# Kernel optimization log

Hardware: AMD Instinct MI355X
Metric: run time of the kernel (lower is better)

The kernel has to match this reference:

```python
import jax, jax.numpy as jnp
import numpy as np

N = 4096
STEPS = 100


def setup_inputs() -> dict:
    key = jax.random.key(0)
    k1, k2 = jax.random.split(key)
    z = jax.random.normal(k1, (N, 2), dtype=jnp.float32) * 0.1  # points in the disc
    K = jax.random.normal(k2, (N, N), dtype=jnp.float32) * 0.1  # coupling matrix param
    omega = jnp.float32(0.1)  # learned natural frequency (scalar)
    dt = jnp.float32(0.05)
    return {"z": z, "K": K, "omega": omega, "dt": dt, "steps": STEPS}


def reference(z, K, omega, dt, steps):
    n = z.shape[0]
    inv2n = 1.0 / (2.0 * n)
    z_c = jax.lax.complex(z[:, 0], z[:, 1])          # (N,) complex64
    K_c = K.astype(jnp.complex64)                    # (N,N) complex (zero imag part)

    def step(zc, _):
        S = K_c @ jnp.conj(zc)                       # (N,)
        T = K_c @ zc                                 # (N,)
        dz = -inv2n * S * zc**2 + omega * zc + inv2n * T
        zc = zc + dt * dz
        a = jnp.abs(zc)
        mask = a >= 0.999
        safe_a = jnp.where(mask, a, 1.0)             # avoid div-by-zero in untaken branch
        zc = jnp.where(mask, zc / safe_a * 0.999, zc)
        return zc, None

    z_c, _ = jax.lax.scan(step, z_c, None, length=steps)

    z_final = jnp.stack([jnp.real(z_c), jnp.imag(z_c)], axis=1)  # (N,2)
    norms = jnp.linalg.norm(z_final, axis=1, keepdims=True)
    mask = norms >= 0.999
    safe_n = jnp.where(mask, norms, 1.0)
    z_final = jnp.where(mask, z_final / safe_n * 0.999, z_final)
    return z_final
```

## Files before the change

### kernel.cpp

```cpp
#include <hip/hip_runtime.h>

#define NN 4096
#define NSTEPS 100
#define TPB 512
#define NBLK 256

__device__ __forceinline__ void zstore_u64(float2* p, unsigned long long u) {
    __hip_atomic_store((unsigned long long*)p, u, __ATOMIC_RELAXED,
                       __HIP_MEMORY_SCOPE_AGENT);
}
__device__ __forceinline__ unsigned long long zload_u64(const float2* p) {
    return __hip_atomic_load((const unsigned long long*)p, __ATOMIC_RELAXED,
                             __HIP_MEMORY_SCOPE_AGENT);
}

__global__ __launch_bounds__(TPB, 2) void k_persist(
    const float* __restrict__ K, const float2* __restrict__ z0,
    float2* __restrict__ zb0, float2* __restrict__ zb1,
    float2* __restrict__ zfinal, const float* __restrict__ omega_p,
    const float* __restrict__ dt_p) {
    __shared__ float P[2][8][68];

    const int tid  = threadIdx.x;
    const int bid  = blockIdx.x;
    const int w    = tid >> 6, lane = tid & 63;
    const int colbase = w * 512 + lane;

    const float omega = *omega_p;
    const float dt    = *dt_p;
    const float inv2n = 1.0f / (2.0f * NN);

    float kA[16][8];
#pragma unroll
    for (int r = 0; r < 16; ++r) {
        const float* Kr = K + (size_t)(bid * 16 + r) * NN + colbase;
#pragma unroll
        for (int j = 0; j < 8; ++j) kA[r][j] = Kr[j * 64];
    }

    float x = 0.f, y = 0.f;
    if ((lane & 31) == 0) {
        float2 zc = z0[bid * 16 + 2 * w + (lane >> 5)];
        x = zc.x; y = zc.y;
    }

    unsigned long long v[8];

    for (int s = 0; s < NSTEPS; ++s) {
#pragma unroll
        for (int r = 0; r < 16; ++r)
#pragma unroll
            for (int j = 0; j < 8; ++j) asm volatile("" : "+v"(kA[r][j]));

        float zre[8], zim[8];
        if (s == 0) {
#pragma unroll
            for (int j = 0; j < 8; ++j) {
                float2 zc = z0[colbase + j * 64];
                zre[j] = zc.x; zim[j] = zc.y;
            }
        } else {
            const float2* zsrc = (s & 1) ? zb1 : zb0;
            const unsigned tag = (unsigned)(s & 7);
            unsigned stale = 0u;
#pragma unroll
            for (int j = 0; j < 8; ++j)
                stale |= (((unsigned)v[j] & 7u) != tag) ? (1u << j) : 0u;
            while (stale) {
                __builtin_amdgcn_s_sleep(1);
#pragma unroll
                for (int j = 0; j < 8; ++j)
                    if (stale & (1u << j))
                        v[j] = zload_u64(zsrc + colbase + j * 64);
#pragma unroll
                for (int j = 0; j < 8; ++j)
                    if ((stale & (1u << j)) && ((unsigned)v[j] & 7u) == tag)
                        stale &= ~(1u << j);
            }
#pragma unroll
            for (int j = 0; j < 8; ++j) {
                union { unsigned u; float f; } cx, cy;
                cx.u = (unsigned)v[j];
                cy.u = (unsigned)(v[j] >> 32);
                zre[j] = cx.f; zim[j] = cy.f;
            }
        }

        float sr[16], si[16];
#pragma unroll
        for (int r = 0; r < 16; ++r) { sr[r] = 0.f; si[r] = 0.f; }
#pragma unroll
        for (int j = 0; j < 8; ++j) {
#pragma unroll
            for (int r = 0; r < 16; ++r) {
                sr[r] += kA[r][j] * zre[j];
                si[r] += kA[r][j] * zim[j];
            }
        }

        if (s + 1 < NSTEPS) {
            const float2* zn = ((s + 1) & 1) ? zb1 : zb0;
#pragma unroll
            for (int j = 0; j < 8; ++j)
                v[j] = zload_u64(zn + colbase + j * 64);
        }

        float a32[32];
#pragma unroll
        for (int r = 0; r < 16; ++r) { a32[r] = sr[r]; a32[16 + r] = si[r]; }
        float b16[16];
#pragma unroll
        for (int m = 0; m < 16; ++m) {
            float aa = a32[2 * m], bb = a32[2 * m + 1];
            bool hi = lane & 1;
            float snd = hi ? aa : bb, kp = hi ? bb : aa;
            b16[m] = kp + __shfl_xor(snd, 1, 64);
        }
        float b8[8];
#pragma unroll
        for (int m = 0; m < 8; ++m) {
            float aa = b16[2 * m], bb = b16[2 * m + 1];
            bool hi = lane & 2;
            float snd = hi ? aa : bb, kp = hi ? bb : aa;
            b8[m] = kp + __shfl_xor(snd, 2, 64);
        }
        float b4[4];
#pragma unroll
        for (int m = 0; m < 4; ++m) {
            float aa = b8[2 * m], bb = b8[2 * m + 1];
            bool hi = lane & 4;
            float snd = hi ? aa : bb, kp = hi ? bb : aa;
            b4[m] = kp + __shfl_xor(snd, 4, 64);
        }
        float b2[2];
#pragma unroll
        for (int m = 0; m < 2; ++m) {
            float aa = b4[2 * m], bb = b4[2 * m + 1];
            bool hi = lane & 8;
            float snd = hi ? aa : bb, kp = hi ? bb : aa;
            b2[m] = kp + __shfl_xor(snd, 8, 64);
        }
        {
            float aa = b2[0], bb = b2[1];
            bool hi = lane & 16;
            float snd = hi ? aa : bb, kp = hi ? bb : aa;
            float red = kp + __shfl_xor(snd, 16, 64);
            P[s & 1][w][lane] = red;
        }
        __syncthreads();

        {
            const int par = s & 1;
            const int r0 = 2 * w, r1 = 2 * w + 1;
            int q    = lane & 7;
            int half = (lane >> 3) & 1;
            int sel  = lane >> 4;
            int rr   = (sel & 2) ? r1 : r0;
            int idx  = ((sel & 1) << 4) + rr;
            float val = P[par][q][half * 32 + idx];
            val += __shfl_xor(val, 1, 64);
            val += __shfl_xor(val, 2, 64);
            val += __shfl_xor(val, 4, 64);
            val += __shfl_xor(val, 8, 64);
            float other = __shfl_xor(val, 16, 64);
            if ((lane & 31) == 0) {
                float u  = val;
                float vv = other;
                float A = x * x - y * y;
                float B = 2.0f * x * y;
                float dzr = inv2n * (u  - (u * A + vv * B)) + omega * x;
                float dzi = inv2n * (vv - (u * B - vv * A)) + omega * y;
                float nx = x + dt * dzr;
                float ny = y + dt * dzi;
                float a2 = nx * nx + ny * ny;
                if (a2 >= 0.999f * 0.999f) {
                    float sc = 0.999f / sqrtf(a2);
                    nx *= sc; ny *= sc;
                }
                x = nx; y = ny;
                int gr = bid * 16 + r0 + (lane >> 5);
                if (s == NSTEPS - 1) {
                    zfinal[gr] = make_float2(nx, ny);
                } else {
                    union { float f; unsigned u; } cx, cy;
                    cx.f = nx; cy.f = ny;
                    cx.u = (cx.u & ~7u) | (unsigned)((s + 1) & 7);
                    unsigned long long pk =
                        (unsigned long long)cx.u |
                        ((unsigned long long)cy.u << 32);
                    float2* zo = ((s + 1) & 1) ? zb1 : zb0;
                    zstore_u64(zo + gr, pk);
                }
            }
        }
    }
}

__global__ __launch_bounds__(256) void k_step_f32(
    const float* __restrict__ K, const float2* __restrict__ zin,
    float2* __restrict__ zout, const float* __restrict__ omega_p,
    const float* __restrict__ dt_p, int n) {
    const int wave = threadIdx.x >> 6;
    const int lane = threadIdx.x & 63;
    const int row  = blockIdx.x * 4 + wave;
    if (row >= n) return;
    float sr = 0.0f, si = 0.0f;
    for (int c = lane; c < n; c += 64) {
        float k = K[(size_t)row * n + c];
        float2 z = zin[c];
        sr += k * z.x;
        si += k * z.y;
    }
#pragma unroll
    for (int off = 32; off; off >>= 1) {
        sr += __shfl_down(sr, off, 64);
        si += __shfl_down(si, off, 64);
    }
    if (lane == 0) {
        float u = sr, v = si;
        float2 zc = zin[row];
        float x = zc.x, y = zc.y;
        float inv2n = 1.0f / (2.0f * n);
        float A = x * x - y * y, B = 2.0f * x * y;
        float dzr = inv2n * (u - (u * A + v * B)) + (*omega_p) * x;
        float dzi = inv2n * (v - (u * B - v * A)) + (*omega_p) * y;
        float nx = x + (*dt_p) * dzr, ny = y + (*dt_p) * dzi;
        float a2 = nx * nx + ny * ny;
        if (a2 >= 0.999f * 0.999f) { float sc = 0.999f / sqrtf(a2); nx *= sc; ny *= sc; }
        zout[row] = make_float2(nx, ny);
    }
}

extern "C" void kernel_launch(void* const* d_in, const int* in_sizes, int n_in,
                              void* d_out, int out_size, void* d_ws, size_t ws_size,
                              hipStream_t stream) {
    const float2* z0      = (const float2*)d_in[0];
    const float*  K       = (const float*)d_in[1];
    const float*  omega_p = (const float*)d_in[2];
    const float*  dt_p    = (const float*)d_in[3];
    const int n = in_sizes[0] / 2;
    float2* out = (float2*)d_out;

    const size_t need = 2 * (size_t)NN * sizeof(float2);
    if (n == NN && ws_size >= need) {
        float2* zb0 = (float2*)d_ws;
        float2* zb1 = zb0 + NN;
        hipMemsetAsync(d_ws, 0, need, stream);
        k_persist<<<NBLK, TPB, 0, stream>>>(K, z0, zb0, zb1, out,
                                            omega_p, dt_p);
    } else {
        float2* zb0 = (float2*)d_ws;
        float2* zb1 = zb0 + n;
        const float2* cur = z0;
        for (int s = 0; s < NSTEPS; ++s) {
            float2* nxt = (s == NSTEPS - 1) ? out : ((s & 1) ? zb1 : zb0);
            k_step_f32<<<(n + 3) / 4, 256, 0, stream>>>(K, cur, nxt, omega_p, dt_p, n);
            cur = nxt;
        }
    }
}
```

Measured before the change: 392.6 us.

## Split persistent kernel across 512 blocks with 8 rows each

Doubles the number of persistent blocks and halves the K rows each block keeps in registers, changing launch bounds to 4 blocks per SM and reshaping the butterfly reduction for 16 partial values. The smaller per-thread register footprint is meant to permit higher occupancy and spread the matvec across more CUs. In exchange, more blocks must poll for the tagged z vector every step, raising global polling traffic and cross-block synchronisation cost. All 512 blocks must also be co-resident or the spin-wait deadlocks.

```diff
diff --git a/kernel.cpp b/kernel.cpp
--- a/kernel.cpp
+++ b/kernel.cpp
@@ -3,7 +3,8 @@
 #define NN 4096
 #define NSTEPS 100
 #define TPB 512
-#define NBLK 256
+#define NBLK 512
+#define NROW 8
 
 __device__ __forceinline__ void zstore_u64(float2* p, unsigned long long u) {
     __hip_atomic_store((unsigned long long*)p, u, __ATOMIC_RELAXED,
@@ -14,12 +15,12 @@
                              __HIP_MEMORY_SCOPE_AGENT);
 }
 
-__global__ __launch_bounds__(TPB, 2) void k_persist(
+__global__ __launch_bounds__(TPB, 4) void k_persist(
     const float* __restrict__ K, const float2* __restrict__ z0,
     float2* __restrict__ zb0, float2* __restrict__ zb1,
     float2* __restrict__ zfinal, const float* __restrict__ omega_p,
     const float* __restrict__ dt_p) {
-    __shared__ float P[2][8][68];
+    __shared__ float P[2][8][17];
 
     const int tid  = threadIdx.x;
     const int bid  = blockIdx.x;
@@ -30,17 +31,17 @@
     const float dt    = *dt_p;
     const float inv2n = 1.0f / (2.0f * NN);
 
-    float kA[16][8];
-#pragma unroll
-    for (int r = 0; r < 16; ++r) {
-        const float* Kr = K + (size_t)(bid * 16 + r) * NN + colbase;
+    float kA[NROW][8];
+#pragma unroll
+    for (int r = 0; r < NROW; ++r) {
+        const float* Kr = K + (size_t)(bid * NROW + r) * NN + colbase;
 #pragma unroll
         for (int j = 0; j < 8; ++j) kA[r][j] = Kr[j * 64];
     }
 
     float x = 0.f, y = 0.f;
-    if ((lane & 31) == 0) {
-        float2 zc = z0[bid * 16 + 2 * w + (lane >> 5)];
+    if (lane == 0) {
+        float2 zc = z0[bid * NROW + w];
         x = zc.x; y = zc.y;
     }
 
@@ -48,7 +49,7 @@
 
     for (int s = 0; s < NSTEPS; ++s) {
 #pragma unroll
-        for (int r = 0; r < 16; ++r)
+        for (int r = 0; r < NROW; ++r)
 #pragma unroll
             for (int j = 0; j < 8; ++j) asm volatile("" : "+v"(kA[r][j]));
 
@@ -86,13 +87,13 @@
             }
         }
 
-        float sr[16], si[16];
-#pragma unroll
-        for (int r = 0; r < 16; ++r) { sr[r] = 0.f; si[r] = 0.f; }
+        float sr[NROW], si[NROW];
+#pragma unroll
+        for (int r = 0; r < NROW; ++r) { sr[r] = 0.f; si[r] = 0.f; }
 #pragma unroll
         for (int j = 0; j < 8; ++j) {
 #pragma unroll
-            for (int r = 0; r < 16; ++r) {
+            for (int r = 0; r < NROW; ++r) {
                 sr[r] += kA[r][j] * zre[j];
                 si[r] += kA[r][j] * zim[j];
             }
@@ -105,65 +106,55 @@
                 v[j] = zload_u64(zn + colbase + j * 64);
         }
 
-        float a32[32];
-#pragma unroll
-        for (int r = 0; r < 16; ++r) { a32[r] = sr[r]; a32[16 + r] = si[r]; }
-        float b16[16];
-#pragma unroll
-        for (int m = 0; m < 16; ++m) {
-            float aa = a32[2 * m], bb = a32[2 * m + 1];
+        float a16[16];
+#pragma unroll
+        for (int r = 0; r < NROW; ++r) { a16[r] = sr[r]; a16[8 + r] = si[r]; }
+        float b8[8];
+#pragma unroll
+        for (int m = 0; m < 8; ++m) {
+            float aa = a16[2 * m], bb = a16[2 * m + 1];
             bool hi = lane & 1;
             float snd = hi ? aa : bb, kp = hi ? bb : aa;
-            b16[m] = kp + __shfl_xor(snd, 1, 64);
-        }
-        float b8[8];
-#pragma unroll
-        for (int m = 0; m < 8; ++m) {
-            float aa = b16[2 * m], bb = b16[2 * m + 1];
-            bool hi = lane & 2;
-            float snd = hi ? aa : bb, kp = hi ? bb : aa;
-            b8[m] = kp + __shfl_xor(snd, 2, 64);
+            b8[m] = kp + __shfl_xor(snd, 1, 64);
         }
         float b4[4];
 #pragma unroll
         for (int m = 0; m < 4; ++m) {
             float aa = b8[2 * m], bb = b8[2 * m + 1];
+            bool hi = lane & 2;
+            float snd = hi ? aa : bb, kp = hi ? bb : aa;
+            b4[m] = kp + __shfl_xor(snd, 2, 64);
+        }
+        float b2[2];
+#pragma unroll
+        for (int m = 0; m < 2; ++m) {
+            float aa = b2[0] * 0.f + b4[2 * m], bb = b4[2 * m + 1];
             bool hi = lane & 4;
             float snd = hi ? aa : bb, kp = hi ? bb : aa;
-            b4[m] = kp + __shfl_xor(snd, 4, 64);
-        }
-        float b2[2];
-#pragma unroll
-        for (int m = 0; m < 2; ++m) {
-            float aa = b4[2 * m], bb = b4[2 * m + 1];
-            bool hi = lane & 8;
-            float snd = hi ? aa : bb, kp = hi ? bb : aa;
-            b2[m] = kp + __shfl_xor(snd, 8, 64);
-        }
+            b2[m] = kp + __shfl_xor(snd, 4, 64);
+        }
+        float red;
         {
             float aa = b2[0], bb = b2[1];
-            bool hi = lane & 16;
-            float snd = hi ? aa : bb, kp = hi ? bb : aa;
-            float red = kp + __shfl_xor(snd, 16, 64);
-            P[s & 1][w][lane] = red;
+            bool hi = lane & 8;
+            float snd = hi ? aa : bb, kp = hi ? bb : aa;
+            red = kp + __shfl_xor(snd, 8, 64);
+            red += __shfl_xor(red, 16, 64);
+            red += __shfl_xor(red, 32, 64);
+            if (lane < 16) P[s & 1][w][lane] = red;
         }
         __syncthreads();
 
         {
             const int par = s & 1;
-            const int r0 = 2 * w, r1 = 2 * w + 1;
-            int q    = lane & 7;
-            int half = (lane >> 3) & 1;
-            int sel  = lane >> 4;
-            int rr   = (sel & 2) ? r1 : r0;
-            int idx  = ((sel & 1) << 4) + rr;
-            float val = P[par][q][half * 32 + idx];
+            int q  = lane & 7;
+            int ri = (lane >> 3) & 1;
+            float val = P[par][q][ri * 8 + w];
             val += __shfl_xor(val, 1, 64);
             val += __shfl_xor(val, 2, 64);
             val += __shfl_xor(val, 4, 64);
-            val += __shfl_xor(val, 8, 64);
-            float other = __shfl_xor(val, 16, 64);
-            if ((lane & 31) == 0) {
+            float other = __shfl_xor(val, 8, 64);
+            if (lane == 0) {
                 float u  = val;
                 float vv = other;
                 float A = x * x - y * y;
@@ -178,7 +169,7 @@
                     nx *= sc; ny *= sc;
                 }
                 x = nx; y = ny;
-                int gr = bid * 16 + r0 + (lane >> 5);
+                int gr = bid * NROW + w;
                 if (s == NSTEPS - 1) {
                     zfinal[gr] = make_float2(nx, ny);
                 } else {
```

New measurement: 913.2 us. 2.33x slower.
